# Kernel tuning notes

Measured on AMD Instinct MI355X. Metric: run time of the kernel, lower is better.

Reference implementation:

```python
import jax, jax.numpy as jnp
import numpy as np
from jax import lax

EPS = 1e-06
PAD = 1


def setup_inputs() -> dict:
    key = jax.random.key(0)
    k1, k2, k3, k4, k5 = jax.random.split(key, 5)
    B, C, H, W = 16, 512, 64, 64  # in_channels == out_channels (required by the module's broadcast)
    w_dim, ksz = 512, 3
    x = jax.random.normal(k1, (B, C, H, W), dtype=jnp.float32)
    w = jax.random.normal(k2, (B, w_dim), dtype=jnp.float32)
    conv_weight = jax.random.normal(k3, (C, C, ksz, ksz), dtype=jnp.float32)
    # nn.Linear(w_dim, out_channels): weight (out, in), bias (out), default uniform init
    bound = 1.0 / np.sqrt(w_dim)
    linear_w = jax.random.uniform(k4, (C, w_dim), minval=-bound, maxval=bound, dtype=jnp.float32)
    linear_b = jax.random.uniform(k5, (C,), minval=-bound, maxval=bound, dtype=jnp.float32)
    return {"x": x, "w": w, "conv_weight": conv_weight, "linear_w": linear_w, "linear_b": linear_b}


def reference(x, w, conv_weight, linear_w, linear_b):
    B, Cin, H, W = x.shape
    # style_scale = Linear(w): (B, out_channels)
    style = jnp.einsum('bd,od->bo', w, linear_w) + linear_b
    # modulate: (1, out, in, k, k) * (B, 1, out, 1, 1)  [requires in == out, as in the source]
    w_prime = conv_weight[None] * style[:, None, :, None, None]
    # demodulate over (in, kh, kw)
    denom = jnp.sqrt(jnp.sum(w_prime ** 2, axis=(2, 3, 4), keepdims=True) + EPS)
    w_pp = w_prime / denom  # (B, out, in, k, k)
    Cout = w_pp.shape[2]
    ksz = w_pp.shape[3]
    # grouped conv trick: fold batch into channels, groups = B
    eff_x = x.reshape(1, B * Cin, H, W)
    eff_f = w_pp.reshape(B * Cout, Cin, ksz, ksz)
    out = lax.conv_general_dilated(
        eff_x, eff_f,
        window_strides=(1, 1),
        padding=[(PAD, PAD), (PAD, PAD)],
        dimension_numbers=('NCHW', 'OIHW', 'NCHW'),
        feature_group_count=B,
    )
    return out.reshape(B, Cout, H, W)
```

## Files before the change

kernel.cpp:

```cpp
#include <hip/hip_runtime.h>

typedef unsigned short ushort_t;
typedef unsigned int uint_t;
typedef __bf16 bf16x8 __attribute__((ext_vector_type(8)));
typedef float float4v __attribute__((ext_vector_type(4)));
typedef uint_t uint4v __attribute__((ext_vector_type(4)));

#define EPS 1e-6f

#define WS_STYLE   0
#define WS_INVD    32768
#define WS_WSQ     65536
#define WS_AW      1114112
#define WS_XP      6291456

__device__ __forceinline__ ushort_t f2bf(float v) {
    union { float f; uint_t u; } c; c.f = v;
    uint_t u = c.u;
    u += 0x7fffu + ((u >> 16) & 1u);
    return (ushort_t)(u >> 16);
}

__device__ __forceinline__ void gload_lds16(const void* g, void* l) {
    __builtin_amdgcn_global_load_lds(
        (const __attribute__((address_space(1))) uint_t*)g,
        (__attribute__((address_space(3))) uint_t*)l, 16, 0, 0);
}

__global__ void compute_style(const float* __restrict__ w, const float* __restrict__ lw,
                              const float* __restrict__ lb, float* __restrict__ style) {
    int gw = blockIdx.x * 4 + (threadIdx.x >> 6);
    int lane = threadIdx.x & 63;
    int b = gw >> 9, o = gw & 511;
    float s = 0.f;
#pragma unroll
    for (int j = 0; j < 8; ++j) {
        int d = j * 64 + lane;
        s += w[b * 512 + d] * lw[o * 512 + d];
    }
#pragma unroll
    for (int off = 32; off; off >>= 1) s += __shfl_down(s, off);
    if (lane == 0) style[gw] = s + lb[o];
}

__global__ void prep_weights(const float* __restrict__ cw, ushort_t* __restrict__ Aw,
                             float* __restrict__ wsq) {
    int id = blockIdx.x * 256 + threadIdx.x;
    int o = id >> 9, i = id & 511;
    const float* p = cw + (size_t)id * 9;
    float s = 0.f;
#pragma unroll
    for (int t = 0; t < 9; ++t) {
        float v = p[t];
        s += v * v;
        Aw[(size_t)o * 4608 + t * 512 + i] = f2bf(v);
    }
    wsq[id] = s;
}

__global__ void compute_invd(const float* __restrict__ wsq, const float* __restrict__ style,
                             float* __restrict__ invd) {
    int gw = blockIdx.x * 4 + (threadIdx.x >> 6);
    int lane = threadIdx.x & 63;
    int b = gw >> 9, o = gw & 511;
    float s = 0.f;
#pragma unroll
    for (int j = 0; j < 8; ++j) {
        int d = j * 64 + lane;
        float st = style[b * 512 + d];
        s += wsq[o * 512 + d] * st * st;
    }
#pragma unroll
    for (int off = 32; off; off >>= 1) s += __shfl_down(s, off);
    if (lane == 0) invd[gw] = rsqrtf(s + EPS);
}

__global__ void zero_border(ushort_t* __restrict__ Xp) {
    int bp = blockIdx.x;
    int b = blockIdx.y;
    int lane = threadIdx.x;
    int py, px;
    if (bp < 66)       { py = 0;        px = bp; }
    else if (bp < 132) { py = 65;       px = bp - 66; }
    else if (bp < 196) { py = bp - 131; px = 0; }
    else               { py = bp - 195; px = 65; }
    size_t pix = ((size_t)b * 66 + py) * 66 + px;
    ((uint4v*)(Xp + pix * 512))[lane] = (uint4v){0, 0, 0, 0};
}

__global__ void modulate_transpose(const float* __restrict__ x, const float* __restrict__ style,
                                   ushort_t* __restrict__ Xp) {
    __shared__ ushort_t tile[64][65];
    int y = blockIdx.x;
    int i0 = blockIdx.y * 64;
    int b = blockIdx.z;
    int tid = threadIdx.x;
    int sub = tid >> 6;
    int lane = tid & 63;
#pragma unroll
    for (int pass = 0; pass < 16; ++pass) {
        int ir = pass * 4 + sub;
        float s = style[b * 512 + i0 + ir];
        float v = x[(((size_t)b * 512 + i0 + ir) * 64 + y) * 64 + lane] * s;
        tile[ir][lane] = f2bf(v);
    }
    __syncthreads();
    size_t rowbase = ((size_t)b * 66 + (y + 1)) * 66 + 1;
#pragma unroll
    for (int pass = 0; pass < 2; ++pass) {
        int idx = pass * 256 + tid;
        int xx = idx >> 3;
        int ch8 = idx & 7;
        ushort_t v[8];
#pragma unroll
        for (int j = 0; j < 8; ++j) v[j] = tile[ch8 * 8 + j][xx];
        *(uint4v*)(Xp + (rowbase + xx) * 512 + i0 + ch8 * 8) = *(uint4v*)v;
    }
}

__global__ __launch_bounds__(512, 2) void conv_gemm(const ushort_t* __restrict__ Aw,
                                                    const ushort_t* __restrict__ Xp,
                                                    const float* __restrict__ invd,
                                                    float* __restrict__ out) {
    __shared__ ushort_t lds[2][32768];

    const int tid  = threadIdx.x;
    const int lane = tid & 63;
    const int wv   = tid >> 6;
    const int wm   = wv >> 2;
    const int wn   = wv & 3;
    const int l15  = lane & 15;
    const int quad = lane >> 4;

    const int bid = blockIdx.x;
    const int lid = (bid & 7) * 64 + (bid >> 3);
    const int pxt = lid & 15;
    const int b   = (lid >> 4) & 15;
    const int ot  = lid >> 8;
    const int o0  = ot * 256;
    const int p0  = pxt * 256;

    const int tr  = tid >> 3;
    const int gsw = (((tid & 7) ^ (tr & 7)) << 4);
    const char* Ab = (const char*)Aw;
    const char* Xb = (const char*)Xp;
    const char* aga[4];
    const char* bga[4];
#pragma unroll
    for (int s = 0; s < 4; ++s) {
        int row = s * 64 + tr;
        aga[s] = Ab + (size_t)(o0 + row) * 9216 + gsw;
        int py0 = pxt * 4 + s;
        bga[s] = Xb + ((size_t)(b * 66 + py0) * 66 + tr) * 1024 + gsw;
    }
    const int lds_wv = wv * 1024;

    const int sw0 = ((quad ^ (l15 & 7)) << 4);
    const int sw1 = (((4 + quad) ^ (l15 & 7)) << 4);
    const int aoffs = (wm * 128 + l15) * 128;
    const int boffs = 32768 + (wn * 64 + l15) * 128;

    float4v acc[8][4] = {};

    auto stage = [&](int kt) {
        const int parity = kt & 1;
        const long aoff = (long)kt * 128;
        const int t = kt >> 3;
        const int dh = t / 3, dw = t - dh * 3;
        const long boff = (long)(dh * 66 + dw) * 1024 + (long)(kt & 7) * 128;
        char* la = (char*)&lds[parity][0]     + lds_wv;
        char* lb = (char*)&lds[parity][16384] + lds_wv;
#pragma unroll
        for (int s = 0; s < 4; ++s) {
            gload_lds16(aga[s] + aoff, la + s * 8192);
            gload_lds16(bga[s] + boff, lb + s * 8192);
        }
    };

    stage(0);
    stage(1);

#pragma unroll 1
    for (int kt = 0; kt < 72; ++kt) {
        if (kt < 71) { asm volatile("s_waitcnt vmcnt(8)" ::: "memory"); }
        else         { asm volatile("s_waitcnt vmcnt(0)" ::: "memory"); }
        __builtin_amdgcn_s_barrier();

        const char* base = (const char*)&lds[kt & 1][0];
        bf16x8 a0[8], a1[8], b0[4], b1[4];
#pragma unroll
        for (int mi = 0; mi < 8; ++mi)
            a0[mi] = *(const bf16x8*)(base + aoffs + mi * 2048 + sw0);
#pragma unroll
        for (int ni = 0; ni < 4; ++ni)
            b0[ni] = *(const bf16x8*)(base + boffs + ni * 2048 + sw0);

        __builtin_amdgcn_s_setprio(1);
#pragma unroll
        for (int mi = 0; mi < 8; ++mi)
#pragma unroll
            for (int ni = 0; ni < 4; ++ni)
                acc[mi][ni] = __builtin_amdgcn_mfma_f32_16x16x32_bf16(a0[mi], b0[ni], acc[mi][ni], 0, 0, 0);
        __builtin_amdgcn_s_setprio(0);

#pragma unroll
        for (int mi = 0; mi < 8; ++mi)
            a1[mi] = *(const bf16x8*)(base + aoffs + mi * 2048 + sw1);
#pragma unroll
        for (int ni = 0; ni < 4; ++ni)
            b1[ni] = *(const bf16x8*)(base + boffs + ni * 2048 + sw1);

        asm volatile("s_waitcnt lgkmcnt(0)" ::: "memory");
        __builtin_amdgcn_s_barrier();

        if (kt < 70) stage(kt + 2);

        __builtin_amdgcn_s_setprio(1);
#pragma unroll
        for (int mi = 0; mi < 8; ++mi)
#pragma unroll
            for (int ni = 0; ni < 4; ++ni)
                acc[mi][ni] = __builtin_amdgcn_mfma_f32_16x16x32_bf16(a1[mi], b1[ni], acc[mi][ni], 0, 0, 0);
        __builtin_amdgcn_s_setprio(0);
    }

    const float* invb = invd + b * 512 + o0 + wm * 128;
    float* outb = out + ((size_t)b * 512 + o0 + wm * 128) * 4096 + p0 + wn * 64;
#pragma unroll
    for (int mi = 0; mi < 8; ++mi) {
#pragma unroll
        for (int r = 0; r < 4; ++r) {
            int m = mi * 16 + quad * 4 + r;
            float d = invb[m];
#pragma unroll
            for (int ni = 0; ni < 4; ++ni) {
                int n = ni * 16 + l15;
                outb[(size_t)m * 4096 + n] = acc[mi][ni][r] * d;
            }
        }
    }
}

extern "C" void kernel_launch(void* const* d_in, const int* in_sizes, int n_in,
                              void* d_out, int out_size, void* d_ws, size_t ws_size,
                              hipStream_t stream) {
    const float* x  = (const float*)d_in[0];
    const float* w  = (const float*)d_in[1];
    const float* cw = (const float*)d_in[2];
    const float* lw = (const float*)d_in[3];
    const float* lb = (const float*)d_in[4];
    float* out = (float*)d_out;

    char* ws = (char*)d_ws;
    float*    style = (float*)(ws + WS_STYLE);
    float*    invd  = (float*)(ws + WS_INVD);
    float*    wsq   = (float*)(ws + WS_WSQ);
    ushort_t* Aw    = (ushort_t*)(ws + WS_AW);
    ushort_t* Xp    = (ushort_t*)(ws + WS_XP);

    compute_style<<<2048, 256, 0, stream>>>(w, lw, lb, style);
    prep_weights<<<1024, 256, 0, stream>>>(cw, Aw, wsq);
    compute_invd<<<2048, 256, 0, stream>>>(wsq, style, invd);
    dim3 gz(260, 16);
    zero_border<<<gz, 64, 0, stream>>>(Xp);
    dim3 g4(64, 8, 16);
    modulate_transpose<<<g4, 256, 0, stream>>>(x, style, Xp);
    conv_gemm<<<512, 512, 0, stream>>>(Aw, Xp, invd, out);
}
```

Before: 502.0 us.

## Fuse prep kernels into two launches, reorder weight K-layout, remap blocks per XCD

Merges the five preprocessing kernels into two multi-role launches: style plus weight prep, then invd plus border zeroing plus modulate-transpose. This cuts launch overhead and inter-kernel gaps. The weight matrix is re-laid out so K runs channel-block-major over the 9 taps, and the GEMM's K-tile-to-tap mapping is changed to match. The block-to-tile mapping now keeps each batch on one XCD so its activation tile gets L2 reuse. The new K ordering touches a different input region each step, which may change cache locality.

Measured after the change: 481.6 us. 4.1% less time.

```diff
diff --git a/kernel.cpp b/kernel.cpp
--- a/kernel.cpp
+++ b/kernel.cpp
@@ -27,94 +27,98 @@
         (__attribute__((address_space(3))) uint_t*)l, 16, 0, 0);
 }
 
-__global__ void compute_style(const float* __restrict__ w, const float* __restrict__ lw,
-                              const float* __restrict__ lb, float* __restrict__ style) {
-    int gw = blockIdx.x * 4 + (threadIdx.x >> 6);
-    int lane = threadIdx.x & 63;
-    int b = gw >> 9, o = gw & 511;
-    float s = 0.f;
-#pragma unroll
-    for (int j = 0; j < 8; ++j) {
-        int d = j * 64 + lane;
-        s += w[b * 512 + d] * lw[o * 512 + d];
-    }
-#pragma unroll
-    for (int off = 32; off; off >>= 1) s += __shfl_down(s, off);
-    if (lane == 0) style[gw] = s + lb[o];
-}
-
-__global__ void prep_weights(const float* __restrict__ cw, ushort_t* __restrict__ Aw,
-                             float* __restrict__ wsq) {
-    int id = blockIdx.x * 256 + threadIdx.x;
-    int o = id >> 9, i = id & 511;
-    const float* p = cw + (size_t)id * 9;
-    float s = 0.f;
-#pragma unroll
-    for (int t = 0; t < 9; ++t) {
-        float v = p[t];
-        s += v * v;
-        Aw[(size_t)o * 4608 + t * 512 + i] = f2bf(v);
-    }
-    wsq[id] = s;
-}
-
-__global__ void compute_invd(const float* __restrict__ wsq, const float* __restrict__ style,
-                             float* __restrict__ invd) {
-    int gw = blockIdx.x * 4 + (threadIdx.x >> 6);
-    int lane = threadIdx.x & 63;
-    int b = gw >> 9, o = gw & 511;
-    float s = 0.f;
-#pragma unroll
-    for (int j = 0; j < 8; ++j) {
-        int d = j * 64 + lane;
-        float st = style[b * 512 + d];
-        s += wsq[o * 512 + d] * st * st;
-    }
-#pragma unroll
-    for (int off = 32; off; off >>= 1) s += __shfl_down(s, off);
-    if (lane == 0) invd[gw] = rsqrtf(s + EPS);
-}
-
-__global__ void zero_border(ushort_t* __restrict__ Xp) {
-    int bp = blockIdx.x;
-    int b = blockIdx.y;
-    int lane = threadIdx.x;
-    int py, px;
-    if (bp < 66)       { py = 0;        px = bp; }
-    else if (bp < 132) { py = 65;       px = bp - 66; }
-    else if (bp < 196) { py = bp - 131; px = 0; }
-    else               { py = bp - 195; px = 65; }
-    size_t pix = ((size_t)b * 66 + py) * 66 + px;
-    ((uint4v*)(Xp + pix * 512))[lane] = (uint4v){0, 0, 0, 0};
-}
-
-__global__ void modulate_transpose(const float* __restrict__ x, const float* __restrict__ style,
-                                   ushort_t* __restrict__ Xp) {
+__global__ void prep_fused1(const float* __restrict__ w, const float* __restrict__ lw,
+                            const float* __restrict__ lb, const float* __restrict__ cw,
+                            float* __restrict__ style, ushort_t* __restrict__ Aw,
+                            float* __restrict__ wsq) {
+    int blk = blockIdx.x;
+    if (blk < 2048) {
+        int gw = blk * 4 + (threadIdx.x >> 6);
+        int lane = threadIdx.x & 63;
+        int b = gw >> 9, o = gw & 511;
+        float s = 0.f;
+#pragma unroll
+        for (int j = 0; j < 8; ++j) {
+            int d = j * 64 + lane;
+            s += w[b * 512 + d] * lw[o * 512 + d];
+        }
+#pragma unroll
+        for (int off = 32; off; off >>= 1) s += __shfl_down(s, off);
+        if (lane == 0) style[gw] = s + lb[o];
+    } else {
+        int id = (blk - 2048) * 256 + threadIdx.x;
+        int o = id >> 9, i = id & 511;
+        const float* p = cw + (size_t)id * 9;
+        size_t base = (size_t)o * 4608 + (size_t)(i >> 6) * 576 + (i & 63);
+        float s = 0.f;
+#pragma unroll
+        for (int t = 0; t < 9; ++t) {
+            float v = p[t];
+            s += v * v;
+            Aw[base + t * 64] = f2bf(v);
+        }
+        wsq[id] = s;
+    }
+}
+
+__global__ void prep_fused2(const float* __restrict__ wsq, const float* __restrict__ style,
+                            float* __restrict__ invd, const float* __restrict__ x,
+                            ushort_t* __restrict__ Xp) {
     __shared__ ushort_t tile[64][65];
-    int y = blockIdx.x;
-    int i0 = blockIdx.y * 64;
-    int b = blockIdx.z;
-    int tid = threadIdx.x;
-    int sub = tid >> 6;
-    int lane = tid & 63;
-#pragma unroll
-    for (int pass = 0; pass < 16; ++pass) {
-        int ir = pass * 4 + sub;
-        float s = style[b * 512 + i0 + ir];
-        float v = x[(((size_t)b * 512 + i0 + ir) * 64 + y) * 64 + lane] * s;
-        tile[ir][lane] = f2bf(v);
-    }
-    __syncthreads();
-    size_t rowbase = ((size_t)b * 66 + (y + 1)) * 66 + 1;
-#pragma unroll
-    for (int pass = 0; pass < 2; ++pass) {
-        int idx = pass * 256 + tid;
-        int xx = idx >> 3;
-        int ch8 = idx & 7;
-        ushort_t v[8];
-#pragma unroll
-        for (int j = 0; j < 8; ++j) v[j] = tile[ch8 * 8 + j][xx];
-        *(uint4v*)(Xp + (rowbase + xx) * 512 + i0 + ch8 * 8) = *(uint4v*)v;
+    int blk = blockIdx.x;
+    if (blk < 2048) {
+        int gw = blk * 4 + (threadIdx.x >> 6);
+        int lane = threadIdx.x & 63;
+        int b = gw >> 9, o = gw & 511;
+        float s = 0.f;
+#pragma unroll
+        for (int j = 0; j < 8; ++j) {
+            int d = j * 64 + lane;
+            float st = style[b * 512 + d];
+            s += wsq[o * 512 + d] * st * st;
+        }
+#pragma unroll
+        for (int off = 32; off; off >>= 1) s += __shfl_down(s, off);
+        if (lane == 0) invd[gw] = rsqrtf(s + EPS);
+    } else if (blk < 3088) {
+        int j = (blk - 2048) * 4 + (threadIdx.x >> 6);
+        int lane = threadIdx.x & 63;
+        int b = j / 260, bp = j - b * 260;
+        int py, px;
+        if (bp < 66)       { py = 0;        px = bp; }
+        else if (bp < 132) { py = 65;       px = bp - 66; }
+        else if (bp < 196) { py = bp - 131; px = 0; }
+        else               { py = bp - 195; px = 65; }
+        size_t pix = ((size_t)b * 66 + py) * 66 + px;
+        ((uint4v*)(Xp + pix * 512))[lane] = (uint4v){0, 0, 0, 0};
+    } else {
+        int mb = blk - 3088;
+        int y = mb & 63;
+        int chunk = mb >> 6;
+        int i0 = (chunk & 7) * 64;
+        int b = chunk >> 3;
+        int tid = threadIdx.x;
+        int sub = tid >> 6;
+        int lane = tid & 63;
+#pragma unroll
+        for (int pass = 0; pass < 16; ++pass) {
+            int ir = pass * 4 + sub;
+            float s = style[b * 512 + i0 + ir];
+            float v = x[(((size_t)b * 512 + i0 + ir) * 64 + y) * 64 + lane] * s;
+            tile[ir][lane] = f2bf(v);
+        }
+        __syncthreads();
+        size_t rowbase = ((size_t)b * 66 + (y + 1)) * 66 + 1;
+#pragma unroll
+        for (int pass = 0; pass < 2; ++pass) {
+            int idx = pass * 256 + tid;
+            int xx = idx >> 3;
+            int ch8 = idx & 7;
+            ushort_t v[8];
+#pragma unroll
+            for (int j = 0; j < 8; ++j) v[j] = tile[ch8 * 8 + j][xx];
+            *(uint4v*)(Xp + (rowbase + xx) * 512 + i0 + ch8 * 8) = *(uint4v*)v;
+        }
     }
 }
 
@@ -133,10 +137,11 @@
     const int quad = lane >> 4;
 
     const int bid = blockIdx.x;
-    const int lid = (bid & 7) * 64 + (bid >> 3);
-    const int pxt = lid & 15;
-    const int b   = (lid >> 4) & 15;
-    const int ot  = lid >> 8;
+    const int xcd = bid & 7;
+    const int ci  = bid >> 3;
+    const int b   = xcd * 2 + (ci >> 5);
+    const int ot  = (ci >> 4) & 1;
+    const int pxt = ci & 15;
     const int o0  = ot * 256;
     const int p0  = pxt * 256;
 
@@ -165,9 +170,10 @@
     auto stage = [&](int kt) {
         const int parity = kt & 1;
         const long aoff = (long)kt * 128;
-        const int t = kt >> 3;
+        const int iblk = (kt * 7282) >> 16;
+        const int t = kt - iblk * 9;
         const int dh = t / 3, dw = t - dh * 3;
-        const long boff = (long)(dh * 66 + dw) * 1024 + (long)(kt & 7) * 128;
+        const long boff = (long)(dh * 66 + dw) * 1024 + (long)iblk * 128;
         char* la = (char*)&lds[parity][0]     + lds_wv;
         char* lb = (char*)&lds[parity][16384] + lds_wv;
 #pragma unroll
@@ -258,12 +264,7 @@
     ushort_t* Aw    = (ushort_t*)(ws + WS_AW);
     ushort_t* Xp    = (ushort_t*)(ws + WS_XP);
 
-    compute_style<<<2048, 256, 0, stream>>>(w, lw, lb, style);
-    prep_weights<<<1024, 256, 0, stream>>>(cw, Aw, wsq);
-    compute_invd<<<2048, 256, 0, stream>>>(wsq, style, invd);
-    dim3 gz(260, 16);
-    zero_border<<<gz, 64, 0, stream>>>(Xp);
-    dim3 g4(64, 8, 16);
-    modulate_transpose<<<g4, 256, 0, stream>>>(x, style, Xp);
+    prep_fused1<<<3072, 256, 0, stream>>>(w, lw, lb, cw, style, Aw, wsq);
+    prep_fused2<<<11280, 256, 0, stream>>>(wsq, style, invd, x, Xp);
     conv_gemm<<<512, 512, 0, stream>>>(Aw, Xp, invd, out);
 }
```
